# Kernel tuning notes

Hardware: AMD Instinct MI355X
Metric: run time of the kernel (lower is better)

Reference implementation:

```python
import jax, jax.numpy as jnp
import numpy as np

H, HK, HD = 6, 2, 128  # n_heads, n_kv_heads, head_dim (from AcousticTransformerArgs defaults)


def setup_inputs() -> dict:
    key = jax.random.key(0)
    k1, k2, k3, k4, k5 = jax.random.split(key, 5)
    B, S, D = 2, 4096, 768
    s = 0.02
    return {
        "x": jax.random.normal(k1, (B, S, D), dtype=jnp.float32),
        "wq": jax.random.normal(k2, (H * HD, D), dtype=jnp.float32) * s,
        "wk": jax.random.normal(k3, (HK * HD, D), dtype=jnp.float32) * s,
        "wv": jax.random.normal(k4, (HK * HD, D), dtype=jnp.float32) * s,
        "wo": jax.random.normal(k5, (D, H * HD), dtype=jnp.float32) * s,
    }


def reference(x, wq, wk, wv, wo):
    B, S, D = x.shape
    rep = H // HK  # GQA repeat factor (3)
    scale = 1.0 / jnp.sqrt(jnp.asarray(HD, x.dtype))
    # projections (torch Linear: y = x @ W^T)
    q = (x @ wq.T).reshape(B, S, HK, rep, HD) * scale  # head h = g*rep + r
    k = (x @ wk.T).reshape(B, S, HK, HD)
    v = (x @ wv.T).reshape(B, S, HK, HD)
    # bidirectional (no mask) attention with GQA broadcast instead of physical repeat
    scores = jnp.einsum("bsgrd,btgd->bgrst", q, k)  # [B,HK,rep,S,S]
    attn = jax.nn.softmax(scores, axis=-1)
    out = jnp.einsum("bgrst,btgd->bsgrd", attn, v).reshape(B, S, H * HD)
    return out @ wo.T
```

## Files before the change

kernel.cpp:

```cpp
#include <hip/hip_runtime.h>
#include <hip/hip_bf16.h>
#include <type_traits>

using bf16 = __hip_bfloat16;
typedef __attribute__((ext_vector_type(8))) short bf16x8;
typedef __attribute__((ext_vector_type(4))) float floatx4;

static constexpr int Bb = 2, S = 4096, D = 768, H = 6, HK = 2, HD = 128, REP = 3;
static constexpr int M_ROWS = Bb * S;
static constexpr int NQKV = 1280;

__device__ __forceinline__ floatx4 mfma16(bf16x8 a, bf16x8 b, floatx4 c) {
  return __builtin_amdgcn_mfma_f32_16x16x32_bf16(a, b, c, 0, 0, 0);
}

__device__ __forceinline__ void gld_lds16(const bf16* g, bf16* l) {
  __builtin_amdgcn_global_load_lds(
      (const __attribute__((address_space(1))) unsigned int*)g,
      (__attribute__((address_space(3))) unsigned int*)l, 16, 0, 0);
}

#if defined(__has_builtin)
#if __has_builtin(__builtin_amdgcn_exp2f)
#define EXP2F(x) __builtin_amdgcn_exp2f(x)
#endif
#endif
#ifndef EXP2F
#define EXP2F(x) exp2f(x)
#endif

__device__ __forceinline__ unsigned pk2(float a, float b) {
  unsigned ua = __builtin_bit_cast(unsigned, a) + 0x8000u;
  unsigned ub = __builtin_bit_cast(unsigned, b) + 0x8000u;
#if defined(__has_builtin) && __has_builtin(__builtin_amdgcn_perm)
  return __builtin_amdgcn_perm(ub, ua, 0x07060302);
#else
  return (ua >> 16) | (ub & 0xffff0000u);
#endif
}

static constexpr size_t E_X  = (size_t)M_ROWS * D;
static constexpr size_t E_WQ = E_X + (size_t)H * HD * D;
static constexpr size_t E_WK = E_WQ + (size_t)HK * HD * D;
static constexpr size_t E_WV = E_WK + (size_t)HK * HD * D;
static constexpr size_t E_WO = E_WV + (size_t)D * H * HD;

__global__ __launch_bounds__(256) void cvt_all(const float* __restrict__ x,
                                               const float* __restrict__ wq,
                                               const float* __restrict__ wk,
                                               const float* __restrict__ wv,
                                               const float* __restrict__ wo,
                                               bf16* __restrict__ xb,
                                               bf16* __restrict__ wqkvb,
                                               bf16* __restrict__ wob, float qscale) {
  size_t i = ((size_t)blockIdx.x * 256 + threadIdx.x) * 4;
  const float* src;
  bf16* dst;
  float s = 1.f;
  size_t off;
  if (i < E_X)        { src = x;  dst = xb;                 off = i; }
  else if (i < E_WQ)  { src = wq; dst = wqkvb;              off = i - E_X; s = qscale; }
  else if (i < E_WK)  { src = wk; dst = wqkvb + 589824;     off = i - E_WQ; }
  else if (i < E_WV)  { src = wv; dst = wqkvb + 786432;     off = i - E_WK; }
  else                { src = wo; dst = wob;                off = i - E_WV; }
  float4 v = *(const float4*)(src + off);
  uint2 st;
  st.x = pk2(v.x * s, v.y * s);
  st.y = pk2(v.z * s, v.w * s);
  *(uint2*)(dst + off) = st;
}

template <typename OutT, bool VT_FUSE>
__global__ __launch_bounds__(256, 3) void gemm_bt(const bf16* __restrict__ A,
                                                  const bf16* __restrict__ W,
                                                  OutT* __restrict__ C,
                                                  bf16* __restrict__ Vt,
                                                  int M, int N, int K) {
  const int tid = threadIdx.x;
  const int wave = tid >> 6, lane = tid & 63;
  const int quad = lane >> 4, lq = lane & 15;
  const int m0 = blockIdx.x * 128, n0 = blockIdx.y * 128;
  const int wm = (wave & 1) * 64, wn = (wave >> 1) * 64;

  __shared__ __align__(16) bf16 As[128 * 64];
  __shared__ __align__(16) bf16 Ws[128 * 64];

  floatx4 acc[4][4] = {};

  const int srow = lane >> 3, sc = lane & 7;

  for (int k0 = 0; k0 < K; k0 += 64) {
#pragma unroll
    for (int i = 0; i < 4; ++i) {
      int ig = wave * 4 + i;
      int r = ig * 8 + srow;
      int c = sc ^ (r & 7);
      gld_lds16(&A[(size_t)(m0 + r) * K + k0 + c * 8], &As[ig * 512]);
      gld_lds16(&W[(size_t)(n0 + r) * K + k0 + c * 8], &Ws[ig * 512]);
    }
    __syncthreads();
#pragma unroll
    for (int kh = 0; kh < 2; ++kh) {
      bf16x8 af[4], wf[4];
#pragma unroll
      for (int i = 0; i < 4; ++i) {
        int ra = wm + i * 16 + lq, rw = wn + i * 16 + lq;
        af[i] = *(const bf16x8*)&As[ra * 64 + (((kh * 4 + quad) ^ (ra & 7)) * 8)];
        wf[i] = *(const bf16x8*)&Ws[rw * 64 + (((kh * 4 + quad) ^ (rw & 7)) * 8)];
      }
#pragma unroll
      for (int i = 0; i < 4; ++i)
#pragma unroll
        for (int j = 0; j < 4; ++j) acc[i][j] = mfma16(af[i], wf[j], acc[i][j]);
    }
    __syncthreads();
  }

  if (VT_FUSE && n0 >= 1024) {
    bf16* tb = (wave < 2 ? As : Ws) + (wave & 1) * 4096;
    char* tc = (char*)tb;
#pragma unroll
    for (int i = 0; i < 4; ++i)
#pragma unroll
      for (int j = 0; j < 4; ++j) {
        uint2 st;
        st.x = pk2(acc[i][j][0], acc[i][j][1]);
        st.y = pk2(acc[i][j][2], acc[i][j][3]);
        int col = j * 16 + lq;
        int cc = (i * 2 + (quad >> 1)) ^ (col & 7);
        *(uint2*)(tc + col * 128 + cc * 16 + (quad & 1) * 8) = st;
      }
    const int b = m0 >> 12;
    const int dd_off = lane >> 3, schunk = lane & 7;
    const int sbase = (m0 & 4095) + wm + schunk * 8;
#pragma unroll
    for (int e = 0; e < 8; ++e) {
      int cl = e * 8 + dd_off;
      int col = (n0 - 1024) + wn + cl;
      int gg = col >> 7, dd = col & 127;
      bf16x8 vv = *(const bf16x8*)(tc + cl * 128 + ((schunk ^ (cl & 7)) * 16));
      *(bf16x8*)&Vt[((size_t)(b * HK + gg) * HD + dd) * S + sbase] = vv;
    }
    return;
  }
#pragma unroll
  for (int i = 0; i < 4; ++i)
#pragma unroll
    for (int j = 0; j < 4; ++j)
#pragma unroll
      for (int r = 0; r < 4; ++r) {
        int row = m0 + wm + i * 16 + quad * 4 + r;
        int col = n0 + wn + j * 16 + lq;
        float v = acc[i][j][r];
        if constexpr (std::is_same_v<OutT, float>)
          C[(size_t)row * N + col] = v;
        else
          C[(size_t)row * N + col] = __float2bfloat16(v);
      }
}

__global__ __launch_bounds__(256, 2) void flash_attn(const bf16* __restrict__ QKV,
                                                     const bf16* __restrict__ Vt,
                                                     bf16* __restrict__ O) {
  const int bid = blockIdx.x;
  const int bg = (bid & 7) >> 1;
  const int b = bg >> 1, g = bg & 1;
  const int qt = ((bid >> 3) << 1) | (bid & 1);
  const int q0 = qt * 32;

  const int tid = threadIdx.x;
  const int w = tid >> 6, lane = tid & 63;
  const int half = w >> 1, wp = w & 1;
  const int quad = lane >> 4, lq = lane & 15;

  __shared__ __align__(16) char smem[77824];
  bf16* Ks = (bf16*)smem;
  bf16* Vs = (bf16*)(smem + 32768);
  bf16* Pt = (bf16*)(smem + 65536);

  const bf16* Kgh = QKV + (size_t)b * S * NQKV + H * HD + g * HD + (size_t)half * 2048 * NQKV;
  const bf16* Vgh = Vt + (size_t)(b * HK + g) * HD * S + half * 2048;

  auto stage = [&](int t0, int buf) {
    bf16* kd = Ks + (buf * 2 + half) * 4096;
    bf16* vd = Vs + (buf * 2 + half) * 4096;
#pragma unroll
    for (int i = 0; i < 4; ++i) {
      int ig = wp * 4 + i;
      int tl = ig * 4 + (lane >> 4);
      int c = (lane & 15) ^ (tl & 15);
      gld_lds16(Kgh + (size_t)(t0 + tl) * NQKV + c * 8, kd + ig * 512);
    }
#pragma unroll
    for (int i = 0; i < 4; ++i) {
      int ig = wp * 4 + i;
      int dl = ig * 16 + (lane >> 2);
      int c = (lane & 3) ^ ((dl >> 1) & 3);
      gld_lds16(Vgh + (size_t)dl * S + t0 + c * 8, vd + ig * 512);
    }
  };

  stage(0, 0);

  const bf16* Qg = QKV + ((size_t)b * S + q0 + wp * 16 + lq) * NQKV + g * REP * HD;
  bf16x8 qf[3][4];
#pragma unroll
  for (int u = 0; u < 3; ++u)
#pragma unroll
    for (int kk = 0; kk < 4; ++kk)
      qf[u][kk] = *(const bf16x8*)(Qg + u * HD + kk * 32 + quad * 8);

  bf16x8 ones;
#pragma unroll
  for (int j = 0; j < 8; ++j) ones[j] = (short)0x3F80;

  floatx4 o[3][8] = {};
  floatx4 lacc[3] = {};
  const int sw = (lq >> 1) & 3;

#pragma unroll 2
  for (int it = 0; it < 64; ++it) {
    const int cur = it & 1;
    __syncthreads();
    if (it + 1 < 64) stage((it + 1) * 32, cur ^ 1);

    const bf16* ks = Ks + (cur * 2 + half) * 4096;
    const bf16* vs = Vs + (cur * 2 + half) * 4096;

    floatx4 sf[3][2] = {};
#pragma unroll
    for (int tt = 0; tt < 2; ++tt)
#pragma unroll
      for (int kk = 0; kk < 4; ++kk) {
        int c = (kk * 4 + quad) ^ lq;
        bf16x8 kf = *(const bf16x8*)&ks[(tt * 16 + lq) * 128 + c * 8];
#pragma unroll
        for (int u = 0; u < 3; ++u) sf[u][tt] = mfma16(kf, qf[u][kk], sf[u][tt]);
      }

#pragma unroll
    for (int u = 0; u < 3; ++u) {
      char* ptb = (char*)(Pt + (w * 3 + u) * 512);
#pragma unroll
      for (int tt = 0; tt < 2; ++tt) {
        float p0 = EXP2F(sf[u][tt][0]), p1 = EXP2F(sf[u][tt][1]);
        float p2 = EXP2F(sf[u][tt][2]), p3 = EXP2F(sf[u][tt][3]);
        uint2 pkv;
        pkv.x = pk2(p0, p1);
        pkv.y = pk2(p2, p3);
        int cc = (tt * 2 + (quad >> 1)) ^ sw;
        *(uint2*)(ptb + lq * 64 + cc * 16 + (quad & 1) * 8) = pkv;
      }
    }

    bf16x8 pf[3];
#pragma unroll
    for (int u = 0; u < 3; ++u) {
      const char* ptb = (const char*)(Pt + (w * 3 + u) * 512);
      pf[u] = *(const bf16x8*)(ptb + lq * 64 + ((quad ^ sw) * 16));
    }

#pragma unroll
    for (int u = 0; u < 3; ++u) lacc[u] = mfma16(ones, pf[u], lacc[u]);

#pragma unroll
    for (int dd = 0; dd < 8; ++dd) {
      bf16x8 vf = *(const bf16x8*)&vs[(dd * 16 + lq) * 32 + ((quad ^ sw) * 8)];
#pragma unroll
      for (int u = 0; u < 3; ++u) o[u][dd] = mfma16(vf, pf[u], o[u][dd]);
    }
  }

  __syncthreads();
  floatx4* oscr = (floatx4*)smem;
  float* lscr = (float*)(smem + 49152);
  if (half == 1) {
#pragma unroll
    for (int u = 0; u < 3; ++u) {
#pragma unroll
      for (int dd = 0; dd < 8; ++dd)
        oscr[((wp * 3 + u) * 8 + dd) * 64 + lane] = o[u][dd];
      lscr[(wp * 3 + u) * 64 + lane] = lacc[u][0];
    }
  }
  __syncthreads();
  if (half == 0) {
    const size_t row = (size_t)b * S + q0 + wp * 16 + lq;
#pragma unroll
    for (int u = 0; u < 3; ++u) {
      float l = lacc[u][0] + lscr[(wp * 3 + u) * 64 + lane];
      float rinv = 1.0f / l;
#pragma unroll
      for (int dd = 0; dd < 8; ++dd) {
        floatx4 oc = o[u][dd] + oscr[((wp * 3 + u) * 8 + dd) * 64 + lane];
        uint2 st;
        st.x = pk2(oc[0] * rinv, oc[1] * rinv);
        st.y = pk2(oc[2] * rinv, oc[3] * rinv);
        int col = (g * REP + u) * HD + dd * 16 + quad * 4;
        *(uint2*)&O[row * (H * HD) + col] = st;
      }
    }
  }
}

static inline size_t al256(size_t x) { return (x + 255) & ~size_t(255); }

extern "C" void kernel_launch(void* const* d_in, const int* in_sizes, int n_in,
                              void* d_out, int out_size, void* d_ws, size_t ws_size,
                              hipStream_t stream) {
  const float* x  = (const float*)d_in[0];
  const float* wq = (const float*)d_in[1];
  const float* wk = (const float*)d_in[2];
  const float* wv = (const float*)d_in[3];
  const float* wo = (const float*)d_in[4];
  float* out = (float*)d_out;

  char* w = (char*)d_ws;
  size_t off = 0;
  auto carve = [&](size_t elems) {
    bf16* p = (bf16*)(w + off);
    off = al256(off + elems * sizeof(bf16));
    return p;
  };
  bf16* xb    = carve((size_t)M_ROWS * D);
  bf16* wqkvb = carve((size_t)NQKV * D);
  bf16* wob   = carve((size_t)D * (H * HD));
  bf16* QKVb  = carve((size_t)M_ROWS * NQKV);
  bf16* Vtb   = carve((size_t)M_ROWS * (HK * HD));
  bf16* Ab    = carve((size_t)M_ROWS * (H * HD));

  const float qscale = 0.1275174465f;

  cvt_all<<<(int)(E_WO / 1024), 256, 0, stream>>>(x, wq, wk, wv, wo, xb, wqkvb, wob, qscale);

  gemm_bt<bf16, true><<<dim3(M_ROWS / 128, NQKV / 128), 256, 0, stream>>>(
      xb, wqkvb, QKVb, Vtb, M_ROWS, NQKV, D);

  flash_attn<<<512, 256, 0, stream>>>(QKVb, Vtb, Ab);

  gemm_bt<float, false><<<dim3(M_ROWS / 128, D / 128), 256, 0, stream>>>(
      Ab, wob, out, nullptr, M_ROWS, D, H * HD);
}
```

Before: 226.8 us.

## Load K/V fragments directly from global into registers, drop LDS staging

Replaces the double-buffered LDS staging of K and V tiles (async global-to-LDS loads plus a block barrier per iteration) with per-wave register prefetch of the next tile's K and V fragments straight from global memory. LDS is now used only for the P transpose and the final cross-half reduction, which shrinks shared memory and removes the per-iteration __syncthreads. The trade-off is that each wave issues its own uncoalesced, strided global loads with no sharing between the waves that need the same K/V rows. The extra prefetch registers also raise register pressure under launch bounds of 2 blocks per CU.

```diff
diff --git a/kernel.cpp b/kernel.cpp
--- a/kernel.cpp
+++ b/kernel.cpp
@@ -173,34 +173,11 @@
   const int half = w >> 1, wp = w & 1;
   const int quad = lane >> 4, lq = lane & 15;
 
-  __shared__ __align__(16) char smem[77824];
-  bf16* Ks = (bf16*)smem;
-  bf16* Vs = (bf16*)(smem + 32768);
-  bf16* Pt = (bf16*)(smem + 65536);
-
-  const bf16* Kgh = QKV + (size_t)b * S * NQKV + H * HD + g * HD + (size_t)half * 2048 * NQKV;
-  const bf16* Vgh = Vt + (size_t)(b * HK + g) * HD * S + half * 2048;
-
-  auto stage = [&](int t0, int buf) {
-    bf16* kd = Ks + (buf * 2 + half) * 4096;
-    bf16* vd = Vs + (buf * 2 + half) * 4096;
-#pragma unroll
-    for (int i = 0; i < 4; ++i) {
-      int ig = wp * 4 + i;
-      int tl = ig * 4 + (lane >> 4);
-      int c = (lane & 15) ^ (tl & 15);
-      gld_lds16(Kgh + (size_t)(t0 + tl) * NQKV + c * 8, kd + ig * 512);
-    }
-#pragma unroll
-    for (int i = 0; i < 4; ++i) {
-      int ig = wp * 4 + i;
-      int dl = ig * 16 + (lane >> 2);
-      int c = (lane & 3) ^ ((dl >> 1) & 3);
-      gld_lds16(Vgh + (size_t)dl * S + t0 + c * 8, vd + ig * 512);
-    }
-  };
-
-  stage(0, 0);
+  __shared__ __align__(16) char smem[62976];
+  bf16* Pt = (bf16*)smem;
+
+  const bf16* Kg = QKV + ((size_t)b * S + half * 2048) * NQKV + H * HD + g * HD;
+  const bf16* Vg = Vt + (size_t)(b * HK + g) * HD * S + half * 2048;
 
   const bf16* Qg = QKV + ((size_t)b * S + q0 + wp * 16 + lq) * NQKV + g * REP * HD;
   bf16x8 qf[3][4];
@@ -213,34 +190,48 @@
   bf16x8 ones;
 #pragma unroll
   for (int j = 0; j < 8; ++j) ones[j] = (short)0x3F80;
+
+  bf16x8 kf[2][4];
+  bf16x8 vf[8];
+
+  auto loadK = [&](int t0) {
+#pragma unroll
+    for (int tt = 0; tt < 2; ++tt)
+#pragma unroll
+      for (int kk = 0; kk < 4; ++kk)
+        kf[tt][kk] =
+            *(const bf16x8*)(Kg + (size_t)(t0 + tt * 16 + lq) * NQKV + kk * 32 + quad * 8);
+  };
+  auto loadV = [&](int t0) {
+#pragma unroll
+    for (int dd = 0; dd < 8; ++dd)
+      vf[dd] = *(const bf16x8*)(Vg + (size_t)(dd * 16 + lq) * S + t0 + quad * 8);
+  };
+
+  loadK(0);
+  loadV(0);
 
   floatx4 o[3][8] = {};
   floatx4 lacc[3] = {};
   const int sw = (lq >> 1) & 3;
-
-#pragma unroll 2
+  char* ptb0 = (char*)(Pt + (w * 3) * 512);
+
   for (int it = 0; it < 64; ++it) {
-    const int cur = it & 1;
-    __syncthreads();
-    if (it + 1 < 64) stage((it + 1) * 32, cur ^ 1);
-
-    const bf16* ks = Ks + (cur * 2 + half) * 4096;
-    const bf16* vs = Vs + (cur * 2 + half) * 4096;
+    const int tn = (it + 1 < 64 ? it + 1 : 63) * 32;
 
     floatx4 sf[3][2] = {};
 #pragma unroll
     for (int tt = 0; tt < 2; ++tt)
 #pragma unroll
-      for (int kk = 0; kk < 4; ++kk) {
-        int c = (kk * 4 + quad) ^ lq;
-        bf16x8 kf = *(const bf16x8*)&ks[(tt * 16 + lq) * 128 + c * 8];
-#pragma unroll
-        for (int u = 0; u < 3; ++u) sf[u][tt] = mfma16(kf, qf[u][kk], sf[u][tt]);
-      }
+      for (int kk = 0; kk < 4; ++kk)
+#pragma unroll
+        for (int u = 0; u < 3; ++u) sf[u][tt] = mfma16(kf[tt][kk], qf[u][kk], sf[u][tt]);
+
+    loadK(tn);
 
 #pragma unroll
     for (int u = 0; u < 3; ++u) {
-      char* ptb = (char*)(Pt + (w * 3 + u) * 512);
+      char* ptb = ptb0 + u * 1024;
 #pragma unroll
       for (int tt = 0; tt < 2; ++tt) {
         float p0 = EXP2F(sf[u][tt][0]), p1 = EXP2F(sf[u][tt][1]);
@@ -255,25 +246,22 @@
 
     bf16x8 pf[3];
 #pragma unroll
-    for (int u = 0; u < 3; ++u) {
-      const char* ptb = (const char*)(Pt + (w * 3 + u) * 512);
-      pf[u] = *(const bf16x8*)(ptb + lq * 64 + ((quad ^ sw) * 16));
-    }
+    for (int u = 0; u < 3; ++u)
+      pf[u] = *(const bf16x8*)(ptb0 + u * 1024 + lq * 64 + ((quad ^ sw) * 16));
 
 #pragma unroll
     for (int u = 0; u < 3; ++u) lacc[u] = mfma16(ones, pf[u], lacc[u]);
 
 #pragma unroll
-    for (int dd = 0; dd < 8; ++dd) {
-      bf16x8 vf = *(const bf16x8*)&vs[(dd * 16 + lq) * 32 + ((quad ^ sw) * 8)];
-#pragma unroll
-      for (int u = 0; u < 3; ++u) o[u][dd] = mfma16(vf, pf[u], o[u][dd]);
-    }
-  }
-
-  __syncthreads();
-  floatx4* oscr = (floatx4*)smem;
-  float* lscr = (float*)(smem + 49152);
+    for (int dd = 0; dd < 8; ++dd)
+#pragma unroll
+      for (int u = 0; u < 3; ++u) o[u][dd] = mfma16(vf[dd], pf[u], o[u][dd]);
+
+    loadV(tn);
+  }
+
+  floatx4* oscr = (floatx4*)(smem + 12288);
+  float* lscr = (float*)(smem + 61440);
   if (half == 1) {
 #pragma unroll
     for (int u = 0; u < 3; ++u) {
```

New measurement: 351.3 us. 1.55x slower.
